# Kernel tuning notes

Hardware: AMD Instinct MI355X
Metric: run time of the kernel (lower is better)

Reference implementation:

```python
import jax, jax.numpy as jnp
import numpy as np

B, S, D, H = 2, 2048, 1024, 16
HD = D // H  # head_dim = 64


def setup_inputs() -> dict:
    key = jax.random.key(0)
    ks = jax.random.split(key, 6)
    scale = 0.02
    return {
        "x": jax.random.normal(ks[0], (B, S, D), dtype=jnp.float32),
        "wq": jax.random.normal(ks[1], (D, D), dtype=jnp.float32) * scale,  # torch Linear weight [out,in]
        "wk": jax.random.normal(ks[2], (D, D), dtype=jnp.float32) * scale,
        "wv": jax.random.normal(ks[3], (D, D), dtype=jnp.float32) * scale,
        "wo": jax.random.normal(ks[4], (D, D), dtype=jnp.float32) * scale,
        "bo": jnp.zeros((D,), dtype=jnp.float32),
    }


def reference(x, wq, wk, wv, wo, bo):
    b, t, d = x.shape
    # projections (torch nn.Linear: x @ W.T), split into heads -> [b, h, t, hd]
    def split_heads(y):
        return y.reshape(b, t, H, HD).transpose(0, 2, 1, 3)

    q = split_heads(x @ wq.T)
    k = split_heads(x @ wk.T)
    v = split_heads(x @ wv.T)

    scores = jnp.einsum("bhqd,bhkd->bhqk", q, k)  # [b,h,t,t]
    causal = jnp.triu(jnp.ones((t, t), dtype=bool), k=1)
    scores = jnp.where(causal, -jnp.inf, scores)
    attn = jax.nn.softmax(scores / jnp.sqrt(jnp.asarray(HD, scores.dtype)), axis=-1)
    # dropout p=0.0 -> identity (eval-mode reference)
    ctx = jnp.einsum("bhqk,bhkd->bhqd", attn, v)
    ctx = ctx.transpose(0, 2, 1, 3).reshape(b, t, d)
    return ctx @ wo.T + bo
```

## Files before the change

kernel.cpp:

```cpp
#include <hip/hip_runtime.h>
#include <stdint.h>
#include <math.h>

#define NH   16
#define HDIM 64
#define SEQ  2048
#define DM   1024
#define NB   2
#define MTOK (NB * SEQ)

typedef __bf16 bf16x8 __attribute__((ext_vector_type(8)));
typedef float  f32x4  __attribute__((ext_vector_type(4)));

__device__ __forceinline__ unsigned short f2bf(float f) {
  union { float f; unsigned int u; } c; c.f = f;
  unsigned int u = c.u;
  return (unsigned short)((u + 0x7FFFu + ((u >> 16) & 1u)) >> 16);
}

__device__ __forceinline__ void async_copy16(const void* g, void* l) {
  __builtin_amdgcn_global_load_lds((__attribute__((address_space(1))) void*)g,
                                   (__attribute__((address_space(3))) void*)l,
                                   16, 0, 0);
}

__global__ void cast_f32_to_bf16(const float* __restrict__ src,
                                 unsigned short* __restrict__ dst, int n4) {
  int i = blockIdx.x * blockDim.x + threadIdx.x;
  if (i >= n4) return;
  float4 v = reinterpret_cast<const float4*>(src)[i];
  ushort4 o;
  o.x = f2bf(v.x); o.y = f2bf(v.y); o.z = f2bf(v.z); o.w = f2bf(v.w);
  reinterpret_cast<ushort4*>(dst)[i] = o;
}

template <int MODE>
__global__ __launch_bounds__(256, 2) void gemm_bt(
    const unsigned short* __restrict__ A,
    const unsigned short* __restrict__ B,
    unsigned short* __restrict__ qo, unsigned short* __restrict__ ko,
    unsigned short* __restrict__ vo,
    float* __restrict__ co, const float* __restrict__ bias,
    int M, int N, int K) {
  __shared__ __align__(16) unsigned short As[128 * 32];
  __shared__ __align__(16) unsigned short Bs[128 * 32];

  const int tid  = threadIdx.x;
  const int lane = tid & 63;
  const int wave = tid >> 6;
  const int l15  = lane & 15;
  const int quad = lane >> 4;
  const int wm   = (wave >> 1) * 64;
  const int wn   = (wave & 1) * 64;
  const int m0   = blockIdx.x * 128;
  const int n0   = blockIdx.y * 128;

  f32x4 acc[4][4];
#pragma unroll
  for (int a = 0; a < 4; ++a)
#pragma unroll
    for (int b = 0; b < 4; ++b) acc[a][b] = f32x4{0.f, 0.f, 0.f, 0.f};

  for (int k0 = 0; k0 < K; k0 += 32) {
    __syncthreads();
#pragma unroll
    for (int s = 0; s < 2; ++s) {
      const int c   = tid + s * 256;
      const int row = c >> 2;
      const int col = (c & 3) * 8;
      unsigned short* lA = As + ((size_t)wave * 64 + s * 256) * 8;
      unsigned short* lB = Bs + ((size_t)wave * 64 + s * 256) * 8;
      async_copy16(A + (size_t)(m0 + row) * K + k0 + col, lA);
      async_copy16(B + (size_t)(n0 + row) * K + k0 + col, lB);
    }
    __syncthreads();

    bf16x8 af[4], bfr[4];
#pragma unroll
    for (int t = 0; t < 4; ++t) {
      af[t]  = *reinterpret_cast<const bf16x8*>(As + (wm + t * 16 + l15) * 32 + quad * 8);
      bfr[t] = *reinterpret_cast<const bf16x8*>(Bs + (wn + t * 16 + l15) * 32 + quad * 8);
    }
#pragma unroll
    for (int ti = 0; ti < 4; ++ti)
#pragma unroll
      for (int tj = 0; tj < 4; ++tj)
        acc[ti][tj] = __builtin_amdgcn_mfma_f32_16x16x32_bf16(af[ti], bfr[tj], acc[ti][tj], 0, 0, 0);
  }

#pragma unroll
  for (int ti = 0; ti < 4; ++ti) {
#pragma unroll
    for (int tj = 0; tj < 4; ++tj) {
      const int mb = m0 + wm + ti * 16 + quad * 4;
      const int n  = n0 + wn + tj * 16 + l15;
      if (MODE == 0) {
        const int which = n >> 10;
        const int n1 = n & 1023;
        const int h = n1 >> 6, d = n1 & 63;
        const int b = mb >> 11, s = mb & 2047;
        if (which == 0) {
          const size_t idx = ((size_t)(b * NH + h) * SEQ + s) * HDIM + d;
#pragma unroll
          for (int r = 0; r < 4; ++r) qo[idx + (size_t)r * HDIM] = f2bf(acc[ti][tj][r] * 0.125f);
        } else if (which == 1) {
          const size_t idx = ((size_t)(b * NH + h) * SEQ + s) * HDIM + d;
#pragma unroll
          for (int r = 0; r < 4; ++r) ko[idx + (size_t)r * HDIM] = f2bf(acc[ti][tj][r]);
        } else {
          const size_t idx = ((size_t)(b * NH + h) * HDIM + d) * SEQ + s;
          ushort4 pk;
          pk.x = f2bf(acc[ti][tj][0]); pk.y = f2bf(acc[ti][tj][1]);
          pk.z = f2bf(acc[ti][tj][2]); pk.w = f2bf(acc[ti][tj][3]);
          *reinterpret_cast<ushort4*>(vo + idx) = pk;
        }
      } else {
#pragma unroll
        for (int r = 0; r < 4; ++r)
          co[(size_t)(mb + r) * N + n] = acc[ti][tj][r] + bias[n];
      }
    }
  }
}

#define KS_STRIDE 80
#define PT_STRIDE 80

__global__ __launch_bounds__(256, 4) void flash_attn_mfma(
    const unsigned short* __restrict__ Qb,
    const unsigned short* __restrict__ Kb,
    const unsigned short* __restrict__ Vtg,
    unsigned short* __restrict__ ctx) {
  __shared__ __align__(16) unsigned short Ks[64 * KS_STRIDE];
  __shared__ __align__(16) unsigned short Vt[64 * KS_STRIDE];
  __shared__ __align__(16) unsigned short Pt[4][16 * PT_STRIDE];

  const int tid  = threadIdx.x;
  const int qt   = gridDim.x - 1 - blockIdx.x;
  const int bh   = blockIdx.y;
  const int q0   = qt * 64;
  const int lane = tid & 63;
  const int wave = tid >> 6;
  const int l15  = lane & 15;
  const int quad = lane >> 4;

  const size_t baseQK = (size_t)bh * SEQ * HDIM;
  const size_t baseV  = (size_t)bh * HDIM * SEQ;

  bf16x8 qf[2];
  {
    const unsigned short* qp = Qb + baseQK + (size_t)(q0 + wave * 16 + l15) * HDIM + quad * 8;
    qf[0] = *reinterpret_cast<const bf16x8*>(qp);
    qf[1] = *reinterpret_cast<const bf16x8*>(qp + 32);
  }

  float m_s = -INFINITY, l_s = 0.f;
  f32x4 o[4];
#pragma unroll
  for (int td = 0; td < 4; ++td) o[td] = f32x4{0.f, 0.f, 0.f, 0.f};

  for (int kt = 0; kt <= qt; ++kt) {
    __syncthreads();
    {
      const int row = tid >> 3;
      const int col = (tid & 7) * 8;
#pragma unroll
      for (int s = 0; s < 2; ++s) {
        const int r2 = row + s * 32;
        const uint4 kv = *reinterpret_cast<const uint4*>(Kb + baseQK + (size_t)(kt * 64 + r2) * HDIM + col);
        const uint4 vv = *reinterpret_cast<const uint4*>(Vtg + baseV + (size_t)r2 * SEQ + kt * 64 + col);
        *reinterpret_cast<uint4*>(&Ks[r2 * KS_STRIDE + col]) = kv;
        *reinterpret_cast<uint4*>(&Vt[r2 * KS_STRIDE + col]) = vv;
      }
    }
    __syncthreads();

    const int tmax = (kt == qt) ? wave : 3;

    f32x4 st[4];
#pragma unroll
    for (int t = 0; t < 4; ++t) st[t] = f32x4{-INFINITY, -INFINITY, -INFINITY, -INFINITY};
#pragma unroll
    for (int t = 0; t < 4; ++t) {
      if (t <= tmax) {
        f32x4 c = f32x4{0.f, 0.f, 0.f, 0.f};
        const bf16x8 kf0 = *reinterpret_cast<const bf16x8*>(&Ks[(t * 16 + l15) * KS_STRIDE + quad * 8]);
        const bf16x8 kf1 = *reinterpret_cast<const bf16x8*>(&Ks[(t * 16 + l15) * KS_STRIDE + 32 + quad * 8]);
        c = __builtin_amdgcn_mfma_f32_16x16x32_bf16(kf0, qf[0], c, 0, 0, 0);
        c = __builtin_amdgcn_mfma_f32_16x16x32_bf16(kf1, qf[1], c, 0, 0, 0);
        if (kt == qt && t == wave) {
#pragma unroll
          for (int r = 0; r < 4; ++r)
            if (quad * 4 + r > l15) c[r] = -INFINITY;
        }
        st[t] = c;
      }
    }

    float mx = -INFINITY;
#pragma unroll
    for (int t = 0; t < 4; ++t)
#pragma unroll
      for (int r = 0; r < 4; ++r) mx = fmaxf(mx, st[t][r]);
    mx = fmaxf(mx, __shfl_xor(mx, 16, 64));
    mx = fmaxf(mx, __shfl_xor(mx, 32, 64));
    const float mnew  = fmaxf(m_s, mx);
    const float alpha = __expf(m_s - mnew);
    m_s = mnew;

    float rs = 0.f;
#pragma unroll
    for (int t = 0; t < 4; ++t) {
      ushort4 pk;
      float p0 = __expf(st[t][0] - mnew);
      float p1 = __expf(st[t][1] - mnew);
      float p2 = __expf(st[t][2] - mnew);
      float p3 = __expf(st[t][3] - mnew);
      rs += (p0 + p1) + (p2 + p3);
      pk.x = f2bf(p0); pk.y = f2bf(p1); pk.z = f2bf(p2); pk.w = f2bf(p3);
      *reinterpret_cast<ushort4*>(&Pt[wave][l15 * PT_STRIDE + t * 16 + quad * 4]) = pk;
    }
    rs += __shfl_xor(rs, 16, 64);
    rs += __shfl_xor(rs, 32, 64);
    l_s = l_s * alpha + rs;

#pragma unroll
    for (int r = 0; r < 4; ++r) {
      const float ar = __shfl(alpha, quad * 4 + r, 64);
#pragma unroll
      for (int td = 0; td < 4; ++td) o[td][r] *= ar;
    }

#pragma unroll
    for (int s = 0; s < 2; ++s) {
      const bf16x8 pf = *reinterpret_cast<const bf16x8*>(&Pt[wave][l15 * PT_STRIDE + s * 32 + quad * 8]);
#pragma unroll
      for (int td = 0; td < 4; ++td) {
        const bf16x8 vf = *reinterpret_cast<const bf16x8*>(&Vt[(td * 16 + l15) * KS_STRIDE + s * 32 + quad * 8]);
        o[td] = __builtin_amdgcn_mfma_f32_16x16x32_bf16(pf, vf, o[td], 0, 0, 0);
      }
    }
  }

  const float linv = 1.f / l_s;
  const int b = bh >> 4, h = bh & 15;
#pragma unroll
  for (int r = 0; r < 4; ++r) {
    const float lr = __shfl(linv, quad * 4 + r, 64);
    const int srow = q0 + wave * 16 + quad * 4 + r;
    const size_t ob = (size_t)(b * SEQ + srow) * DM + h * HDIM + l15;
#pragma unroll
    for (int td = 0; td < 4; ++td)
      ctx[ob + td * 16] = f2bf(o[td][r] * lr);
  }
}

extern "C" void kernel_launch(void* const* d_in, const int* in_sizes, int n_in,
                              void* d_out, int out_size, void* d_ws, size_t ws_size,
                              hipStream_t stream) {
  const float* x  = (const float*)d_in[0];
  const float* wq = (const float*)d_in[1];
  const float* wk = (const float*)d_in[2];
  const float* wv = (const float*)d_in[3];
  const float* wo = (const float*)d_in[4];
  const float* bo = (const float*)d_in[5];
  float* out = (float*)d_out;

  char* ws = (char*)d_ws;
  unsigned short* xb    = (unsigned short*)(ws);
  unsigned short* wqkvb = (unsigned short*)(ws + (8ull  << 20));
  unsigned short* wob   = (unsigned short*)(ws + (14ull << 20));
  unsigned short* Qb    = (unsigned short*)(ws + (16ull << 20));
  unsigned short* Kb    = (unsigned short*)(ws + (24ull << 20));
  unsigned short* Vtg   = (unsigned short*)(ws + (32ull << 20));
  unsigned short* ctxb  = (unsigned short*)(ws + (40ull << 20));

  cast_f32_to_bf16<<<4096, 256, 0, stream>>>(x,  xb,                  MTOK * DM / 4);
  cast_f32_to_bf16<<<1024, 256, 0, stream>>>(wq, wqkvb,               DM * DM / 4);
  cast_f32_to_bf16<<<1024, 256, 0, stream>>>(wk, wqkvb + DM * DM,     DM * DM / 4);
  cast_f32_to_bf16<<<1024, 256, 0, stream>>>(wv, wqkvb + 2 * DM * DM, DM * DM / 4);
  cast_f32_to_bf16<<<1024, 256, 0, stream>>>(wo, wob,                 DM * DM / 4);

  dim3 g1(MTOK / 128, (3 * DM) / 128);
  gemm_bt<0><<<g1, 256, 0, stream>>>(xb, wqkvb, Qb, Kb, Vtg, nullptr, nullptr,
                                     MTOK, 3 * DM, DM);

  dim3 g2(SEQ / 64, NB * NH);
  flash_attn_mfma<<<g2, 256, 0, stream>>>(Qb, Kb, Vtg, ctxb);

  dim3 g3(MTOK / 128, DM / 128);
  gemm_bt<1><<<g3, 256, 0, stream>>>(ctxb, wob, nullptr, nullptr, nullptr, out, bo,
                                     MTOK, DM, DM);
}
```

Baseline: 221.4 us.

## Process two query sub-tiles per attention block and merge cast kernels

```diff
diff --git a/kernel.cpp b/kernel.cpp
--- a/kernel.cpp
+++ b/kernel.cpp
@@ -24,9 +24,22 @@
                                    16, 0, 0);
 }
 
-__global__ void cast_f32_to_bf16(const float* __restrict__ src,
-                                 unsigned short* __restrict__ dst, int n4) {
-  int i = blockIdx.x * blockDim.x + threadIdx.x;
+__global__ void cast_all(const float* __restrict__ x,  const float* __restrict__ wq,
+                         const float* __restrict__ wk, const float* __restrict__ wv,
+                         const float* __restrict__ wo,
+                         unsigned short* __restrict__ xb,
+                         unsigned short* __restrict__ wqkvb,
+                         unsigned short* __restrict__ wob) {
+  const int seg = blockIdx.y;
+  const float* src;
+  unsigned short* dst;
+  int n4;
+  if (seg == 0)      { src = x;  dst = xb;                  n4 = MTOK * DM / 4; }
+  else if (seg == 1) { src = wq; dst = wqkvb;               n4 = DM * DM / 4; }
+  else if (seg == 2) { src = wk; dst = wqkvb + DM * DM;     n4 = DM * DM / 4; }
+  else if (seg == 3) { src = wv; dst = wqkvb + 2 * DM * DM; n4 = DM * DM / 4; }
+  else               { src = wo; dst = wob;                 n4 = DM * DM / 4; }
+  const int i = blockIdx.x * blockDim.x + threadIdx.x;
   if (i >= n4) return;
   float4 v = reinterpret_cast<const float4*>(src)[i];
   ushort4 o;
@@ -126,19 +139,19 @@
 #define KS_STRIDE 80
 #define PT_STRIDE 80
 
-__global__ __launch_bounds__(256, 4) void flash_attn_mfma(
+__global__ __launch_bounds__(256, 3) void flash_attn_mfma(
     const unsigned short* __restrict__ Qb,
     const unsigned short* __restrict__ Kb,
     const unsigned short* __restrict__ Vtg,
     unsigned short* __restrict__ ctx) {
   __shared__ __align__(16) unsigned short Ks[64 * KS_STRIDE];
   __shared__ __align__(16) unsigned short Vt[64 * KS_STRIDE];
-  __shared__ __align__(16) unsigned short Pt[4][16 * PT_STRIDE];
+  __shared__ __align__(16) unsigned short Pt[4][2][16 * PT_STRIDE];
 
   const int tid  = threadIdx.x;
   const int qt   = gridDim.x - 1 - blockIdx.x;
   const int bh   = blockIdx.y;
-  const int q0   = qt * 64;
+  const int q0   = qt * 128;
   const int lane = tid & 63;
   const int wave = tid >> 6;
   const int l15  = lane & 15;
@@ -147,19 +160,25 @@
   const size_t baseQK = (size_t)bh * SEQ * HDIM;
   const size_t baseV  = (size_t)bh * HDIM * SEQ;
 
-  bf16x8 qf[2];
-  {
-    const unsigned short* qp = Qb + baseQK + (size_t)(q0 + wave * 16 + l15) * HDIM + quad * 8;
-    qf[0] = *reinterpret_cast<const bf16x8*>(qp);
-    qf[1] = *reinterpret_cast<const bf16x8*>(qp + 32);
-  }
-
-  float m_s = -INFINITY, l_s = 0.f;
-  f32x4 o[4];
-#pragma unroll
-  for (int td = 0; td < 4; ++td) o[td] = f32x4{0.f, 0.f, 0.f, 0.f};
-
-  for (int kt = 0; kt <= qt; ++kt) {
+  bf16x8 qf[2][2];
+#pragma unroll
+  for (int sp = 0; sp < 2; ++sp) {
+    const unsigned short* qp =
+        Qb + baseQK + (size_t)(q0 + sp * 64 + wave * 16 + l15) * HDIM + quad * 8;
+    qf[sp][0] = *reinterpret_cast<const bf16x8*>(qp);
+    qf[sp][1] = *reinterpret_cast<const bf16x8*>(qp + 32);
+  }
+
+  float m_s[2] = {-INFINITY, -INFINITY};
+  float l_s[2] = {0.f, 0.f};
+  f32x4 o[2][4];
+#pragma unroll
+  for (int sp = 0; sp < 2; ++sp)
+#pragma unroll
+    for (int td = 0; td < 4; ++td) o[sp][td] = f32x4{0.f, 0.f, 0.f, 0.f};
+
+  const int ktmax = 2 * qt + 1;
+  for (int kt = 0; kt <= ktmax; ++kt) {
     __syncthreads();
     {
       const int row = tid >> 3;
@@ -175,83 +194,113 @@
     }
     __syncthreads();
 
-    const int tmax = (kt == qt) ? wave : 3;
-
-    f32x4 st[4];
-#pragma unroll
-    for (int t = 0; t < 4; ++t) st[t] = f32x4{-INFINITY, -INFINITY, -INFINITY, -INFINITY};
+    const int rel0 = ((q0 + wave * 16) >> 4) - kt * 4;
+    const int rel1 = rel0 + 4;
+
+    f32x4 st[2][4];
+#pragma unroll
+    for (int sp = 0; sp < 2; ++sp)
+#pragma unroll
+      for (int t = 0; t < 4; ++t)
+        st[sp][t] = f32x4{-INFINITY, -INFINITY, -INFINITY, -INFINITY};
+
 #pragma unroll
     for (int t = 0; t < 4; ++t) {
-      if (t <= tmax) {
-        f32x4 c = f32x4{0.f, 0.f, 0.f, 0.f};
+      if (t <= rel1) {
         const bf16x8 kf0 = *reinterpret_cast<const bf16x8*>(&Ks[(t * 16 + l15) * KS_STRIDE + quad * 8]);
         const bf16x8 kf1 = *reinterpret_cast<const bf16x8*>(&Ks[(t * 16 + l15) * KS_STRIDE + 32 + quad * 8]);
-        c = __builtin_amdgcn_mfma_f32_16x16x32_bf16(kf0, qf[0], c, 0, 0, 0);
-        c = __builtin_amdgcn_mfma_f32_16x16x32_bf16(kf1, qf[1], c, 0, 0, 0);
-        if (kt == qt && t == wave) {
-#pragma unroll
-          for (int r = 0; r < 4; ++r)
-            if (quad * 4 + r > l15) c[r] = -INFINITY;
+        if (t <= rel0) {
+          f32x4 c = f32x4{0.f, 0.f, 0.f, 0.f};
+          c = __builtin_amdgcn_mfma_f32_16x16x32_bf16(kf0, qf[0][0], c, 0, 0, 0);
+          c = __builtin_amdgcn_mfma_f32_16x16x32_bf16(kf1, qf[0][1], c, 0, 0, 0);
+          if (t == rel0) {
+#pragma unroll
+            for (int r = 0; r < 4; ++r)
+              if (quad * 4 + r > l15) c[r] = -INFINITY;
+          }
+          st[0][t] = c;
         }
-        st[t] = c;
-      }
-    }
-
-    float mx = -INFINITY;
-#pragma unroll
-    for (int t = 0; t < 4; ++t)
-#pragma unroll
-      for (int r = 0; r < 4; ++r) mx = fmaxf(mx, st[t][r]);
-    mx = fmaxf(mx, __shfl_xor(mx, 16, 64));
-    mx = fmaxf(mx, __shfl_xor(mx, 32, 64));
-    const float mnew  = fmaxf(m_s, mx);
-    const float alpha = __expf(m_s - mnew);
-    m_s = mnew;
-
-    float rs = 0.f;
-#pragma unroll
-    for (int t = 0; t < 4; ++t) {
-      ushort4 pk;
-      float p0 = __expf(st[t][0] - mnew);
-      float p1 = __expf(st[t][1] - mnew);
-      float p2 = __expf(st[t][2] - mnew);
-      float p3 = __expf(st[t][3] - mnew);
-      rs += (p0 + p1) + (p2 + p3);
-      pk.x = f2bf(p0); pk.y = f2bf(p1); pk.z = f2bf(p2); pk.w = f2bf(p3);
-      *reinterpret_cast<ushort4*>(&Pt[wave][l15 * PT_STRIDE + t * 16 + quad * 4]) = pk;
-    }
-    rs += __shfl_xor(rs, 16, 64);
-    rs += __shfl_xor(rs, 32, 64);
-    l_s = l_s * alpha + rs;
-
-#pragma unroll
-    for (int r = 0; r < 4; ++r) {
-      const float ar = __shfl(alpha, quad * 4 + r, 64);
-#pragma unroll
-      for (int td = 0; td < 4; ++td) o[td][r] *= ar;
-    }
-
+        {
+          f32x4 c = f32x4{0.f, 0.f, 0.f, 0.f};
+          c = __builtin_amdgcn_mfma_f32_16x16x32_bf16(kf0, qf[1][0], c, 0, 0, 0);
+          c = __builtin_amdgcn_mfma_f32_16x16x32_bf16(kf1, qf[1][1], c, 0, 0, 0);
+          if (t == rel1) {
+#pragma unroll
+            for (int r = 0; r < 4; ++r)
+              if (quad * 4 + r > l15) c[r] = -INFINITY;
+          }
+          st[1][t] = c;
+        }
+      }
+    }
+
+#pragma unroll
+    for (int sp = 0; sp < 2; ++sp) {
+      const int rel = sp ? rel1 : rel0;
+      if (rel < 0) continue;
+      float mx = -INFINITY;
+#pragma unroll
+      for (int t = 0; t < 4; ++t)
+#pragma unroll
+        for (int r = 0; r < 4; ++r) mx = fmaxf(mx, st[sp][t][r]);
+      mx = fmaxf(mx, __shfl_xor(mx, 16, 64));
+      mx = fmaxf(mx, __shfl_xor(mx, 32, 64));
+      const float mnew  = fmaxf(m_s[sp], mx);
+      const float alpha = __expf(m_s[sp] - mnew);
+      m_s[sp] = mnew;
+
+      float rs = 0.f;
+#pragma unroll
+      for (int t = 0; t < 4; ++t) {
+        ushort4 pk;
+        const float p0 = __expf(st[sp][t][0] - mnew);
+        const float p1 = __expf(st[sp][t][1] - mnew);
+        const float p2 = __expf(st[sp][t][2] - mnew);
+        const float p3 = __expf(st[sp][t][3] - mnew);
+        rs += (p0 + p1) + (p2 + p3);
+        pk.x = f2bf(p0); pk.y = f2bf(p1); pk.z = f2bf(p2); pk.w = f2bf(p3);
+        *reinterpret_cast<ushort4*>(&Pt[wave][sp][l15 * PT_STRIDE + t * 16 + quad * 4]) = pk;
+      }
+      rs += __shfl_xor(rs, 16, 64);
+      rs += __shfl_xor(rs, 32, 64);
+      l_s[sp] = l_s[sp] * alpha + rs;
+
+#pragma unroll
+      for (int r = 0; r < 4; ++r) {
+        const float ar = __shfl(alpha, quad * 4 + r, 64);
+#pragma unroll
+        for (int td = 0; td < 4; ++td) o[sp][td][r] *= ar;
+      }
+    }
+
+    const bool s0 = (rel0 >= 0);
 #pragma unroll
     for (int s = 0; s < 2; ++s) {
-      const bf16x8 pf = *reinterpret_cast<const bf16x8*>(&Pt[wave][l15 * PT_STRIDE + s * 32 + quad * 8]);
+      bf16x8 pf0, pf1;
+      if (s0) pf0 = *reinterpret_cast<const bf16x8*>(&Pt[wave][0][l15 * PT_STRIDE + s * 32 + quad * 8]);
+      pf1 = *reinterpret_cast<const bf16x8*>(&Pt[wave][1][l15 * PT_STRIDE + s * 32 + quad * 8]);
 #pragma unroll
       for (int td = 0; td < 4; ++td) {
         const bf16x8 vf = *reinterpret_cast<const bf16x8*>(&Vt[(td * 16 + l15) * KS_STRIDE + s * 32 + quad * 8]);
-        o[td] = __builtin_amdgcn_mfma_f32_16x16x32_bf16(pf, vf, o[td], 0, 0, 0);
-      }
-    }
-  }
-
-  const float linv = 1.f / l_s;
+        if (s0) o[0][td] = __builtin_amdgcn_mfma_f32_16x16x32_bf16(pf0, vf, o[0][td], 0, 0, 0);
+        o[1][td] = __builtin_amdgcn_mfma_f32_16x16x32_bf16(pf1, vf, o[1][td], 0, 0, 0);
+      }
+    }
+  }
+
   const int b = bh >> 4, h = bh & 15;
 #pragma unroll
-  for (int r = 0; r < 4; ++r) {
-    const float lr = __shfl(linv, quad * 4 + r, 64);
-    const int srow = q0 + wave * 16 + quad * 4 + r;
-    const size_t ob = (size_t)(b * SEQ + srow) * DM + h * HDIM + l15;
-#pragma unroll
-    for (int td = 0; td < 4; ++td)
-      ctx[ob + td * 16] = f2bf(o[td][r] * lr);
+  for (int sp = 0; sp < 2; ++sp) {
+    const float linv = 1.f / l_s[sp];
+#pragma unroll
+    for (int r = 0; r < 4; ++r) {
+      const float lr = __shfl(linv, quad * 4 + r, 64);
+      const int srow = q0 + sp * 64 + wave * 16 + quad * 4 + r;
+      const size_t ob = (size_t)(b * SEQ + srow) * DM + h * HDIM + l15;
+#pragma unroll
+      for (int td = 0; td < 4; ++td)
+        ctx[ob + td * 16] = f2bf(o[sp][td][r] * lr);
+    }
   }
 }
 
@@ -275,17 +324,14 @@
   unsigned short* Vtg   = (unsigned short*)(ws + (32ull << 20));
   unsigned short* ctxb  = (unsigned short*)(ws + (40ull << 20));
 
-  cast_f32_to_bf16<<<4096, 256, 0, stream>>>(x,  xb,                  MTOK * DM / 4);
-  cast_f32_to_bf16<<<1024, 256, 0, stream>>>(wq, wqkvb,               DM * DM / 4);
-  cast_f32_to_bf16<<<1024, 256, 0, stream>>>(wk, wqkvb + DM * DM,     DM * DM / 4);
-  cast_f32_to_bf16<<<1024, 256, 0, stream>>>(wv, wqkvb + 2 * DM * DM, DM * DM / 4);
-  cast_f32_to_bf16<<<1024, 256, 0, stream>>>(wo, wob,                 DM * DM / 4);
+  dim3 gc(4096, 5);
+  cast_all<<<gc, 256, 0, stream>>>(x, wq, wk, wv, wo, xb, wqkvb, wob);
 
   dim3 g1(MTOK / 128, (3 * DM) / 128);
   gemm_bt<0><<<g1, 256, 0, stream>>>(xb, wqkvb, Qb, Kb, Vtg, nullptr, nullptr,
                                      MTOK, 3 * DM, DM);
 
-  dim3 g2(SEQ / 64, NB * NH);
+  dim3 g2(SEQ / 128, NB * NH);
   flash_attn_mfma<<<g2, 256, 0, stream>>>(Qb, Kb, Vtg, ctxb);
 
   dim3 g3(MTOK / 128, DM / 128);
```

Result: slower. 232.7 us (+5.1%).
